# Kernel optimization log

Hardware: AMD Instinct MI355X
Metric: run time of the kernel (lower is better)

The kernel has to match this reference:

```python
import jax, jax.numpy as jnp
import numpy as np

N = 100000
NFEAT = 128
NHID = 16
HEADS = 8
NCLASS = 40
E = 1600000
NEG_SLOPE = 0.2  # PyG GATConv default


def glorot(key, shape):
    fan = shape[0] + shape[-1]
    limit = float(np.sqrt(6.0 / fan))
    return jax.random.uniform(key, shape, jnp.float32, -limit, limit)


def setup_inputs() -> dict:
    key = jax.random.key(0)
    ks = jax.random.split(key, 10)
    x = jax.random.normal(ks[0], (N, NFEAT), jnp.float32)
    adj = jnp.zeros((1,), jnp.float32)  # unused by forward, kept for signature parity
    edge_index = jax.random.randint(ks[1], (2, E), 0, N, jnp.int64)
    # layer 1: GATConv(NFEAT, NHID, heads=HEADS)
    W1 = glorot(ks[2], (NFEAT, HEADS * NHID))
    att_src1 = glorot(ks[3], (HEADS, NHID))
    att_dst1 = glorot(ks[4], (HEADS, NHID))
    b1 = jnp.zeros((HEADS * NHID,), jnp.float32)
    # layer 2: GATConv(HEADS*NHID, NCLASS, heads=1)
    W2 = glorot(ks[5], (HEADS * NHID, NCLASS))
    att_src2 = glorot(ks[6], (1, NCLASS))
    att_dst2 = glorot(ks[7], (1, NCLASS))
    b2 = jnp.zeros((NCLASS,), jnp.float32)
    return {"x": x, "adj": adj, "edge_index": edge_index,
            "W1": W1, "att_src1": att_src1, "att_dst1": att_dst1, "b1": b1,
            "W2": W2, "att_src2": att_src2, "att_dst2": att_dst2, "b2": b2}


def gat_conv(x, W, att_src, att_dst, bias, src, dst, heads, out_ch):
    n = x.shape[0]
    h = (x @ W).reshape(n, heads, out_ch)              # [N,H,C]
    a_src = (h * att_src[None]).sum(-1)                # [N,H]
    a_dst = (h * att_dst[None]).sum(-1)                # [N,H]
    e = jax.nn.leaky_relu(a_src[src] + a_dst[dst], NEG_SLOPE)  # [E,H]
    # softmax over incoming edges of each destination node
    m = jax.ops.segment_max(e, dst, num_segments=n)
    e = jnp.exp(e - m[dst])
    s = jax.ops.segment_sum(e, dst, num_segments=n)
    alpha = e / s[dst]                                  # [E,H]
    msg = h[src] * alpha[:, :, None]                    # [E,H,C]
    out = jax.ops.segment_sum(msg, dst, num_segments=n)  # [N,H,C]
    return out.reshape(n, heads * out_ch) + bias


def reference(x, adj, edge_index, W1, att_src1, att_dst1, b1, W2, att_src2, att_dst2, b2):
    # PyG GATConv adds self-loops by default
    loops = jnp.arange(N, dtype=edge_index.dtype)
    src = jnp.concatenate([edge_index[0], loops])
    dst = jnp.concatenate([edge_index[1], loops])
    # eval mode: F.dropout is identity
    h = jax.nn.elu(gat_conv(x, W1, att_src1, att_dst1, b1, src, dst, HEADS, NHID))
    h = jax.nn.elu(gat_conv(h, W2, att_src2, att_dst2, b2, src, dst, 1, NCLASS))
    return jax.nn.log_softmax(h, axis=1)
```

## Files before the change

### kernel.cpp

```cpp
#include <hip/hip_runtime.h>
#include <stdint.h>

#define NEG_SLOPE 0.2f

__device__ __forceinline__ float lrelu(float v) { return v >= 0.f ? v : NEG_SLOPE * v; }
__device__ __forceinline__ float elu(float v) { return v > 0.f ? v : expm1f(v); }
__device__ __forceinline__ float pexp(float v) { return __expf(lrelu(v)); }

typedef _Float16 h16x2 __attribute__((ext_vector_type(2)));
typedef _Float16 half8 __attribute__((ext_vector_type(8)));
typedef float floatx4 __attribute__((ext_vector_type(4)));

__device__ __forceinline__ void fma_h2(float& a0, float& a1, float p, unsigned u) {
    h16x2 h = __builtin_bit_cast(h16x2, u);
    a0 += p * (float)h[0];
    a1 += p * (float)h[1];
}


#define HC 1024

__global__ __launch_bounds__(256) void hist_wt_kernel(const int* __restrict__ ei,
                                                      int* __restrict__ deg,
                                                      unsigned* __restrict__ rankd,
                                                      const float* __restrict__ W1,
                                                      const float* __restrict__ W2,
                                                      _Float16* __restrict__ w1t,
                                                      _Float16* __restrict__ w2t,
                                                      int E, int n, int sz) {
    const int b = blockIdx.x;
    const int tid = threadIdx.x;
    if (b < 64) {
        int t = b * 256 + tid;
        int col = t >> 7, k = t & 127;
        w1t[col * 128 + k] = (_Float16)W1[k * 128 + col];
        return;
    }
    if (b < 88) {
        int t = (b - 64) * 256 + tid;
        if (t < 48 * 128) {
            int col = t >> 7, k = t & 127;
            w2t[t] = (col < 40) ? (_Float16)W2[k * 40 + col] : (_Float16)0.f;
        }
        return;
    }
    const int hb = b - 88;
    const int c = hb >> 3, r = hb & 7;
    const int lo = r * sz;
    const int hi = (lo + sz < n) ? lo + sz : n;
    const bool last = (r == 7);
    const int base = c * HC;
    #pragma unroll
    for (int i = 0; i < 4; i++) {
        int e = base + i * 256 + tid;
        if (e >= E) break;
        int d = ei[E + e];
        if (d >= lo && d < hi) {
            unsigned rk = (unsigned)atomicAdd(&deg[d], 1);
            rankd[e] = ((unsigned)d << 7) | rk;
        } else if (last && (unsigned)d >= (unsigned)n) {
            rankd[e] = 0xFFFFFFFFu;
        }
    }
}


#define SCAN_T 256
#define SCAN_TILE 1024

__global__ __launch_bounds__(SCAN_T) void scan_p1_kernel(const int* __restrict__ deg,
                                                         int* __restrict__ bsum, int n) {
    __shared__ int red[SCAN_T];
    int t = threadIdx.x;
    int base = blockIdx.x * SCAN_TILE + t * 4;
    int s = 0;
    #pragma unroll
    for (int i = 0; i < 4; i++) {
        int idx = base + i;
        if (idx < n) s += deg[idx];
    }
    red[t] = s;
    __syncthreads();
    for (int off = SCAN_T / 2; off; off >>= 1) {
        if (t < off) red[t] += red[t + off];
        __syncthreads();
    }
    if (t == 0) bsum[blockIdx.x] = red[0];
}

__global__ __launch_bounds__(SCAN_T) void scan_p3f_kernel(const int* __restrict__ deg,
                                                          const int* __restrict__ bsum,
                                                          int* __restrict__ row_ptr,
                                                          int n, int nbk) {
    __shared__ int red[SCAN_T];
    int t = threadIdx.x;
    red[t] = (t < nbk && t < blockIdx.x) ? bsum[t] : 0;
    __syncthreads();
    for (int off = SCAN_T / 2; off; off >>= 1) {
        if (t < off) red[t] += red[t + off];
        __syncthreads();
    }
    const int blockoff = red[0];
    __syncthreads();

    int base = blockIdx.x * SCAN_TILE + t * 4;
    int v[4];
    int s = 0;
    #pragma unroll
    for (int i = 0; i < 4; i++) {
        int idx = base + i;
        v[i] = (idx < n) ? deg[idx] : 0;
        s += v[i];
    }
    red[t] = s;
    __syncthreads();
    for (int off = 1; off < SCAN_T; off <<= 1) {
        int add = (t >= off) ? red[t - off] : 0;
        __syncthreads();
        red[t] += add;
        __syncthreads();
    }
    int excl = red[t] - s + blockoff;
    #pragma unroll
    for (int i = 0; i < 4; i++) {
        int idx = base + i;
        if (idx < n) row_ptr[idx] = excl;
        excl += v[i];
        if (idx == n - 1) row_ptr[n] = excl;
    }
}

__global__ void scatter_kernel(const int* __restrict__ ei, const unsigned* __restrict__ rankd,
                               const int* __restrict__ row_ptr,
                               int* __restrict__ csr_src, int E) {
    int e = blockIdx.x * blockDim.x + threadIdx.x;
    if (e >= E) return;
    unsigned rd = rankd[e];
    if (rd == 0xFFFFFFFFu) return;
    csr_src[row_ptr[rd >> 7] + (int)(rd & 127u)] = ei[e];
}


__global__ __launch_bounds__(256) void gemm1_mfma_kernel(
    const float* __restrict__ x, const _Float16* __restrict__ w1t,
    const float* __restrict__ as1, const float* __restrict__ ad1,
    _Float16* __restrict__ h1h, float* __restrict__ a1s, float* __restrict__ a1d, int n) {
    __shared__ __align__(16) char Wl[32768];
    const int tid = threadIdx.x;
    {
        const uint4* Wg = (const uint4*)w1t;
        #pragma unroll
        for (int i = 0; i < 8; i++) {
            int it = tid + i * 256;
            uint4 v = Wg[it];
            int b = it * 16;
            *(uint4*)&Wl[b ^ (((b >> 8) & 7) << 4)] = v;
        }
    }
    const int wave = tid >> 6, lane = tid & 63;
    const int cl = lane & 15, g = lane >> 4;
    const int wbase = blockIdx.x * 64 + wave * 16;

    int arow = wbase + cl;
    if (arow >= n) arow = n - 1;
    half8 afr[4];
    #pragma unroll
    for (int t = 0; t < 4; t++) {
        const float4 v0 = *(const float4*)&x[(size_t)arow * 128 + 32 * t + g * 8];
        const float4 v1 = *(const float4*)&x[(size_t)arow * 128 + 32 * t + g * 8 + 4];
        afr[t][0] = (_Float16)v0.x; afr[t][1] = (_Float16)v0.y;
        afr[t][2] = (_Float16)v0.z; afr[t][3] = (_Float16)v0.w;
        afr[t][4] = (_Float16)v1.x; afr[t][5] = (_Float16)v1.y;
        afr[t][6] = (_Float16)v1.z; afr[t][7] = (_Float16)v1.w;
    }
    __syncthreads();

    #pragma unroll
    for (int ct = 0; ct < 8; ct++) {
        const int col = ct * 16 + cl;
        half8 bfr[4];
        #pragma unroll
        for (int t = 0; t < 4; t++) {
            int b = (col << 8) + 64 * t + 16 * g;
            bfr[t] = *(half8*)&Wl[b ^ ((col & 7) << 4)];
        }
        floatx4 acc = {0.f, 0.f, 0.f, 0.f};
        #pragma unroll
        for (int t = 0; t < 4; t++)
            acc = __builtin_amdgcn_mfma_f32_16x16x32_f16(afr[t], bfr[t], acc, 0, 0, 0);
        const float av = as1[col], dv = ad1[col];
        #pragma unroll
        for (int i = 0; i < 4; i++) {
            int r = wbase + g * 4 + i;
            float hv = acc[i];
            if (r < n) h1h[(size_t)r * 128 + col] = (_Float16)hv;
            float ps = hv * av, pd = hv * dv;
            ps += __shfl_xor(ps, 1); ps += __shfl_xor(ps, 2);
            ps += __shfl_xor(ps, 4); ps += __shfl_xor(ps, 8);
            pd += __shfl_xor(pd, 1); pd += __shfl_xor(pd, 2);
            pd += __shfl_xor(pd, 4); pd += __shfl_xor(pd, 8);
            if (cl == 0 && r < n) {
                a1s[r * 8 + ct] = ps;
                a1d[r * 8 + ct] = pd;
            }
        }
    }
}

__global__ __launch_bounds__(256) void agg1_kernel(const int* __restrict__ row_ptr,
                                                   const int* __restrict__ csr_src,
                                                   const float* __restrict__ a1s,
                                                   const float* __restrict__ a1d,
                                                   const uint4* __restrict__ h1q,
                                                   const float* __restrict__ b1,
                                                   _Float16* __restrict__ h2h, int n) {
    int lane = threadIdx.x & 63;
    int d = blockIdx.x * 4 + (threadIdx.x >> 6);
    if (d >= n) return;
    const int g = lane >> 4;
    const int q = lane & 15;
    const int h = q >> 1;
    const float adh = a1d[d * 8 + h];

    float acc[8];
    #pragma unroll
    for (int i = 0; i < 8; i++) acc[i] = 0.f;
    float sum = 0.f;
    if (g == 0) {
        uint4 w = h1q[(size_t)d * 16 + q];
        float ps = pexp(a1s[d * 8 + h] + adh);
        fma_h2(acc[0], acc[1], ps, w.x);
        fma_h2(acc[2], acc[3], ps, w.y);
        fma_h2(acc[4], acc[5], ps, w.z);
        fma_h2(acc[6], acc[7], ps, w.w);
        sum = ps;
    }
    int beg = row_ptr[d], end = row_ptr[d + 1];
    int e = beg + g;
    for (; e + 12 < end; e += 16) {
        int s0 = csr_src[e],     s1 = csr_src[e + 4];
        int s2 = csr_src[e + 8], s3 = csr_src[e + 12];
        uint4 w0 = h1q[(size_t)s0 * 16 + q];
        uint4 w1 = h1q[(size_t)s1 * 16 + q];
        uint4 w2 = h1q[(size_t)s2 * 16 + q];
        uint4 w3 = h1q[(size_t)s3 * 16 + q];
        float p0 = pexp(a1s[s0 * 8 + h] + adh);
        float p1 = pexp(a1s[s1 * 8 + h] + adh);
        float p2 = pexp(a1s[s2 * 8 + h] + adh);
        float p3 = pexp(a1s[s3 * 8 + h] + adh);
        fma_h2(acc[0], acc[1], p0, w0.x); fma_h2(acc[2], acc[3], p0, w0.y);
        fma_h2(acc[4], acc[5], p0, w0.z); fma_h2(acc[6], acc[7], p0, w0.w);
        fma_h2(acc[0], acc[1], p1, w1.x); fma_h2(acc[2], acc[3], p1, w1.y);
        fma_h2(acc[4], acc[5], p1, w1.z); fma_h2(acc[6], acc[7], p1, w1.w);
        fma_h2(acc[0], acc[1], p2, w2.x); fma_h2(acc[2], acc[3], p2, w2.y);
        fma_h2(acc[4], acc[5], p2, w2.z); fma_h2(acc[6], acc[7], p2, w2.w);
        fma_h2(acc[0], acc[1], p3, w3.x); fma_h2(acc[2], acc[3], p3, w3.y);
        fma_h2(acc[4], acc[5], p3, w3.z); fma_h2(acc[6], acc[7], p3, w3.w);
        sum += (p0 + p1) + (p2 + p3);
    }
    for (; e + 4 < end; e += 8) {
        int s0 = csr_src[e], s1 = csr_src[e + 4];
        uint4 w0 = h1q[(size_t)s0 * 16 + q];
        uint4 w1 = h1q[(size_t)s1 * 16 + q];
        float p0 = pexp(a1s[s0 * 8 + h] + adh);
        float p1 = pexp(a1s[s1 * 8 + h] + adh);
        fma_h2(acc[0], acc[1], p0, w0.x); fma_h2(acc[2], acc[3], p0, w0.y);
        fma_h2(acc[4], acc[5], p0, w0.z); fma_h2(acc[6], acc[7], p0, w0.w);
        fma_h2(acc[0], acc[1], p1, w1.x); fma_h2(acc[2], acc[3], p1, w1.y);
        fma_h2(acc[4], acc[5], p1, w1.z); fma_h2(acc[6], acc[7], p1, w1.w);
        sum += p0 + p1;
    }
    for (; e < end; e += 4) {
        int s = csr_src[e];
        uint4 w = h1q[(size_t)s * 16 + q];
        float p = pexp(a1s[s * 8 + h] + adh);
        fma_h2(acc[0], acc[1], p, w.x);
        fma_h2(acc[2], acc[3], p, w.y);
        fma_h2(acc[4], acc[5], p, w.z);
        fma_h2(acc[6], acc[7], p, w.w);
        sum += p;
    }
    sum += __shfl_xor(sum, 16); sum += __shfl_xor(sum, 32);
    #pragma unroll
    for (int i = 0; i < 8; i++) {
        acc[i] += __shfl_xor(acc[i], 16);
        acc[i] += __shfl_xor(acc[i], 32);
    }
    if (g == 0) {
        float rs = 1.f / sum;
        float4 b0 = *(const float4*)&b1[8 * q];
        float4 b4 = *(const float4*)&b1[8 * q + 4];
        half8 o;
        o[0] = (_Float16)elu(acc[0] * rs + b0.x);
        o[1] = (_Float16)elu(acc[1] * rs + b0.y);
        o[2] = (_Float16)elu(acc[2] * rs + b0.z);
        o[3] = (_Float16)elu(acc[3] * rs + b0.w);
        o[4] = (_Float16)elu(acc[4] * rs + b4.x);
        o[5] = (_Float16)elu(acc[5] * rs + b4.y);
        o[6] = (_Float16)elu(acc[6] * rs + b4.z);
        o[7] = (_Float16)elu(acc[7] * rs + b4.w);
        *(half8*)&h2h[(size_t)d * 128 + 8 * q] = o;
    }
}


__global__ __launch_bounds__(256) void gemm2_mfma_kernel(
    const _Float16* __restrict__ h2h, const _Float16* __restrict__ w2t,
    const float* __restrict__ as2, const float* __restrict__ ad2,
    _Float16* __restrict__ h3pk, float* __restrict__ a2d, int n) {
    const int tid = threadIdx.x;
    const int wave = tid >> 6, lane = tid & 63;
    const int cl = lane & 15, g = lane >> 4;
    const int wbase = blockIdx.x * 64 + wave * 16;

    int arow = wbase + cl;
    if (arow >= n) arow = n - 1;
    half8 afr[4];
    #pragma unroll
    for (int t = 0; t < 4; t++)
        afr[t] = *(const half8*)&h2h[(size_t)arow * 128 + 32 * t + 8 * g];

    float ps[4] = {0.f, 0.f, 0.f, 0.f};
    float pd[4] = {0.f, 0.f, 0.f, 0.f};
    #pragma unroll
    for (int ct = 0; ct < 3; ct++) {
        const int col = ct * 16 + cl;
        half8 bfr[4];
        #pragma unroll
        for (int t = 0; t < 4; t++)
            bfr[t] = *(const half8*)&w2t[col * 128 + 32 * t + 8 * g];
        floatx4 acc = {0.f, 0.f, 0.f, 0.f};
        #pragma unroll
        for (int t = 0; t < 4; t++)
            acc = __builtin_amdgcn_mfma_f32_16x16x32_f16(afr[t], bfr[t], acc, 0, 0, 0);
        const bool cv = (col < 40);
        const float av = cv ? as2[col] : 0.f;
        const float dv = cv ? ad2[col] : 0.f;
        #pragma unroll
        for (int i = 0; i < 4; i++) {
            int r = wbase + g * 4 + i;
            float hv = acc[i];
            if (cv && r < n)
                h3pk[(size_t)r * 64 + 2 + col] = (_Float16)hv;
            ps[i] += hv * av;
            pd[i] += hv * dv;
        }
    }
    #pragma unroll
    for (int i = 0; i < 4; i++) {
        float s = ps[i], dd = pd[i];
        s += __shfl_xor(s, 1); s += __shfl_xor(s, 2);
        s += __shfl_xor(s, 4); s += __shfl_xor(s, 8);
        dd += __shfl_xor(dd, 1); dd += __shfl_xor(dd, 2);
        dd += __shfl_xor(dd, 4); dd += __shfl_xor(dd, 8);
        int r = wbase + g * 4 + i;
        if (cl == 0 && r < n) {
            ((float*)h3pk)[(size_t)r * 32] = s;
            a2d[r] = dd;
        }
    }
}

__global__ __launch_bounds__(256) void agg2_final_kernel(const int* __restrict__ row_ptr,
                                                         const int* __restrict__ csr_src,
                                                         const unsigned* __restrict__ h3u,
                                                         const float* __restrict__ a2d,
                                                         const float* __restrict__ b2,
                                                         float* __restrict__ out, int n) {
    const float* h3a = (const float*)h3u;
    int lane = threadIdx.x & 63;
    int d = blockIdx.x * 4 + (threadIdx.x >> 6);
    if (d >= n) return;
    const int g = lane >> 5;
    const int q = lane & 31;
    const bool act = (q < 20);
    const float adh = a2d[d];

    h16x2 hsel = {(_Float16)0.f, (_Float16)0.f};
    if (act && g == 0) hsel = __builtin_bit_cast(h16x2, h3u[(size_t)d * 32 + 1 + q]);

    float acc0 = 0.f, acc1 = 0.f, sum = 0.f;
    if (g == 0) {
        float ps = pexp(h3a[(size_t)d * 32] + adh);
        acc0 = ps * (float)hsel[0]; acc1 = ps * (float)hsel[1]; sum = ps;
    }
    int beg = row_ptr[d], end = row_ptr[d + 1];
    int e = beg + g;
    for (; e + 6 < end; e += 8) {
        int s0 = csr_src[e],     s1 = csr_src[e + 2];
        int s2 = csr_src[e + 4], s3 = csr_src[e + 6];
        float a0 = h3a[(size_t)s0 * 32], a1 = h3a[(size_t)s1 * 32];
        float a2 = h3a[(size_t)s2 * 32], a3 = h3a[(size_t)s3 * 32];
        unsigned w0 = 0u, w1 = 0u, w2 = 0u, w3 = 0u;
        if (act) {
            w0 = h3u[(size_t)s0 * 32 + 1 + q]; w1 = h3u[(size_t)s1 * 32 + 1 + q];
            w2 = h3u[(size_t)s2 * 32 + 1 + q]; w3 = h3u[(size_t)s3 * 32 + 1 + q];
        }
        float p0 = pexp(a0 + adh), p1 = pexp(a1 + adh);
        float p2 = pexp(a2 + adh), p3 = pexp(a3 + adh);
        fma_h2(acc0, acc1, p0, w0);
        fma_h2(acc0, acc1, p1, w1);
        fma_h2(acc0, acc1, p2, w2);
        fma_h2(acc0, acc1, p3, w3);
        sum += (p0 + p1) + (p2 + p3);
    }
    for (; e + 2 < end; e += 4) {
        int s0 = csr_src[e], s1 = csr_src[e + 2];
        float a0 = h3a[(size_t)s0 * 32], a1 = h3a[(size_t)s1 * 32];
        unsigned w0 = 0u, w1 = 0u;
        if (act) {
            w0 = h3u[(size_t)s0 * 32 + 1 + q];
            w1 = h3u[(size_t)s1 * 32 + 1 + q];
        }
        float p0 = pexp(a0 + adh), p1 = pexp(a1 + adh);
        fma_h2(acc0, acc1, p0, w0);
        fma_h2(acc0, acc1, p1, w1);
        sum += p0 + p1;
    }
    for (; e < end; e += 2) {
        int s = csr_src[e];
        float pe = pexp(h3a[(size_t)s * 32] + adh);
        unsigned w = act ? h3u[(size_t)s * 32 + 1 + q] : 0u;
        fma_h2(acc0, acc1, pe, w);
        sum += pe;
    }
    sum += __shfl_xor(sum, 32);
    acc0 += __shfl_xor(acc0, 32);
    acc1 += __shfl_xor(acc1, 32);

    float rs = 1.f / sum;
    float v0 = -3.0e38f, v1 = -3.0e38f;
    if (act) {
        v0 = elu(acc0 * rs + b2[2 * q]);
        v1 = elu(acc1 * rs + b2[2 * q + 1]);
    }
    float mx = (act && g == 0) ? fmaxf(v0, v1) : -3.0e38f;
    #pragma unroll
    for (int off = 32; off; off >>= 1) mx = fmaxf(mx, __shfl_xor(mx, off, 64));
    float es = (act && g == 0) ? (__expf(v0 - mx) + __expf(v1 - mx)) : 0.f;
    #pragma unroll
    for (int off = 32; off; off >>= 1) es += __shfl_xor(es, off, 64);
    if (act && g == 0) {
        float ls = logf(es);
        float2 o;
        o.x = v0 - mx - ls;
        o.y = v1 - mx - ls;
        *(float2*)&out[(size_t)d * 40 + 2 * q] = o;
    }
}

extern "C" void kernel_launch(void* const* d_in, const int* in_sizes, int n_in,
                              void* d_out, int out_size, void* d_ws, size_t ws_size,
                              hipStream_t stream) {
    const float* x   = (const float*)d_in[0];
    const int*   ei  = (const int*)d_in[2];
    const float* W1  = (const float*)d_in[3];
    const float* as1 = (const float*)d_in[4];
    const float* ad1 = (const float*)d_in[5];
    const float* b1  = (const float*)d_in[6];
    const float* W2  = (const float*)d_in[7];
    const float* as2 = (const float*)d_in[8];
    const float* ad2 = (const float*)d_in[9];
    const float* b2  = (const float*)d_in[10];
    float* out = (float*)d_out;

    const int n = in_sizes[0] / 128;
    const int E = in_sizes[2] / 2;
    const int nb = (n + SCAN_TILE - 1) / SCAN_TILE;
    const int nbc = (E + HC - 1) / HC;
    const int sz = (n + 7) / 8;

    float* ws = (float*)d_ws;
    _Float16* h1h = (_Float16*)ws;
    _Float16* h2h = (_Float16*)(ws + (size_t)n * 64);
    float* A  = ws + (size_t)n * 128;
    int* deg    = (int*)A;
    int* bsum   = deg + n;
    float* a1s = A;
    float* a1d = A + (size_t)n * 8;
    float* a2d = A;
    int* row_ptr = (int*)(A + (size_t)n * 16);
    int* csr_src = row_ptr + (n + 1);
    unsigned* rankd = (unsigned*)(csr_src + E);
    _Float16* w1t = (_Float16*)(((uintptr_t)(rankd + E) + 63) & ~(uintptr_t)63);
    _Float16* w2t = w1t + 128 * 128;
    _Float16* h3pk = h1h;

    hipMemsetAsync(deg, 0, (size_t)n * sizeof(int), stream);
    hist_wt_kernel<<<88 + nbc * 8, 256, 0, stream>>>(ei, deg, rankd, W1, W2,
                                                     w1t, w2t, E, n, sz);
    scan_p1_kernel<<<nb, SCAN_T, 0, stream>>>(deg, bsum, n);
    scan_p3f_kernel<<<nb, SCAN_T, 0, stream>>>(deg, bsum, row_ptr, n, nb);
    scatter_kernel<<<(E + 255) / 256, 256, 0, stream>>>(ei, rankd, row_ptr, csr_src, E);

    gemm1_mfma_kernel<<<(n + 63) / 64, 256, 0, stream>>>(x, w1t, as1, ad1, h1h, a1s, a1d, n);
    agg1_kernel<<<(n + 3) / 4, 256, 0, stream>>>(row_ptr, csr_src, a1s, a1d,
                                                 (const uint4*)h1h, b1, h2h, n);

    gemm2_mfma_kernel<<<(n + 63) / 64, 256, 0, stream>>>(h2h, w2t, as2, ad2, h3pk, a2d, n);
    agg2_final_kernel<<<(n + 3) / 4, 256, 0, stream>>>(row_ptr, csr_src, (const unsigned*)h3pk,
                                                       a2d, b2, out, n);
}
```

Measured before the change: 413.3 us.

## Move destination-range partitioning from histogram to CSR scatter kernel

The histogram kernel now processes each edge once with a plain atomicAdd instead of eight passes partitioned by destination range. The scatter kernel instead takes the 8-way destination partitioning, with each block reading four edges through vector loads and writing only those whose destination falls in its slice. This is meant to improve the locality of the row_ptr gathers and csr_src writes, and to shrink the histogram launch. The cost is that the scatter now reads rankd and ei eight times, atomics in the histogram lose range locality, and the vector loads assume E is a multiple of 4 (rankd is realigned to 16 bytes for this).

Result: no change. 413.4 us (+0.0%).

```diff
diff --git a/kernel.cpp b/kernel.cpp
--- a/kernel.cpp
+++ b/kernel.cpp
@@ -17,8 +17,6 @@
     a1 += p * (float)h[1];
 }
 
-
-#define HC 1024
 
 __global__ __launch_bounds__(256) void hist_wt_kernel(const int* __restrict__ ei,
                                                       int* __restrict__ deg,
@@ -27,7 +25,7 @@
                                                       const float* __restrict__ W2,
                                                       _Float16* __restrict__ w1t,
                                                       _Float16* __restrict__ w2t,
-                                                      int E, int n, int sz) {
+                                                      int E, int n) {
     const int b = blockIdx.x;
     const int tid = threadIdx.x;
     if (b < 64) {
@@ -44,24 +42,13 @@
         }
         return;
     }
-    const int hb = b - 88;
-    const int c = hb >> 3, r = hb & 7;
-    const int lo = r * sz;
-    const int hi = (lo + sz < n) ? lo + sz : n;
-    const bool last = (r == 7);
-    const int base = c * HC;
-    #pragma unroll
-    for (int i = 0; i < 4; i++) {
-        int e = base + i * 256 + tid;
-        if (e >= E) break;
-        int d = ei[E + e];
-        if (d >= lo && d < hi) {
-            unsigned rk = (unsigned)atomicAdd(&deg[d], 1);
-            rankd[e] = ((unsigned)d << 7) | rk;
-        } else if (last && (unsigned)d >= (unsigned)n) {
-            rankd[e] = 0xFFFFFFFFu;
-        }
-    }
+    int e = (b - 88) * 256 + tid;
+    if (e >= E) return;
+    int d = ei[E + e];
+    unsigned rd = 0xFFFFFFFFu;
+    if ((unsigned)d < (unsigned)n)
+        rd = ((unsigned)d << 7) | (unsigned)atomicAdd(&deg[d], 1);
+    rankd[e] = rd;
 }
 
 
@@ -130,14 +117,34 @@
     }
 }
 
-__global__ void scatter_kernel(const int* __restrict__ ei, const unsigned* __restrict__ rankd,
-                               const int* __restrict__ row_ptr,
-                               int* __restrict__ csr_src, int E) {
-    int e = blockIdx.x * blockDim.x + threadIdx.x;
-    if (e >= E) return;
-    unsigned rd = rankd[e];
-    if (rd == 0xFFFFFFFFu) return;
-    csr_src[row_ptr[rd >> 7] + (int)(rd & 127u)] = ei[e];
+
+#define SC 1024
+
+__global__ __launch_bounds__(256) void scatter8_kernel(const int* __restrict__ ei,
+                                                       const unsigned* __restrict__ rankd,
+                                                       const int* __restrict__ row_ptr,
+                                                       int* __restrict__ csr_src,
+                                                       int E, int sz) {
+    const int hb = blockIdx.x;
+    const int c = hb >> 3, r = hb & 7;
+    const int lo = r * sz, hi = lo + sz;
+    int e0 = c * SC + threadIdx.x * 4;
+    if (e0 >= E) return;
+    uint4 r4 = *(const uint4*)&rankd[e0];
+    int4 s4 = *(const int4*)&ei[e0];
+    int d;
+    d = (int)(r4.x >> 7);
+    if (r4.x != 0xFFFFFFFFu && d >= lo && d < hi)
+        csr_src[row_ptr[d] + (int)(r4.x & 127u)] = s4.x;
+    d = (int)(r4.y >> 7);
+    if (r4.y != 0xFFFFFFFFu && d >= lo && d < hi)
+        csr_src[row_ptr[d] + (int)(r4.y & 127u)] = s4.y;
+    d = (int)(r4.z >> 7);
+    if (r4.z != 0xFFFFFFFFu && d >= lo && d < hi)
+        csr_src[row_ptr[d] + (int)(r4.z & 127u)] = s4.z;
+    d = (int)(r4.w >> 7);
+    if (r4.w != 0xFFFFFFFFu && d >= lo && d < hi)
+        csr_src[row_ptr[d] + (int)(r4.w & 127u)] = s4.w;
 }
 
 
@@ -467,7 +474,8 @@
     const int n = in_sizes[0] / 128;
     const int E = in_sizes[2] / 2;
     const int nb = (n + SCAN_TILE - 1) / SCAN_TILE;
-    const int nbc = (E + HC - 1) / HC;
+    const int nbh = (E + 255) / 256;
+    const int nsc = (E + SC - 1) / SC;
     const int sz = (n + 7) / 8;
 
     float* ws = (float*)d_ws;
@@ -481,17 +489,17 @@
     float* a2d = A;
     int* row_ptr = (int*)(A + (size_t)n * 16);
     int* csr_src = row_ptr + (n + 1);
-    unsigned* rankd = (unsigned*)(csr_src + E);
+    unsigned* rankd = (unsigned*)(((uintptr_t)(csr_src + E) + 15) & ~(uintptr_t)15);
     _Float16* w1t = (_Float16*)(((uintptr_t)(rankd + E) + 63) & ~(uintptr_t)63);
     _Float16* w2t = w1t + 128 * 128;
     _Float16* h3pk = h1h;
 
     hipMemsetAsync(deg, 0, (size_t)n * sizeof(int), stream);
-    hist_wt_kernel<<<88 + nbc * 8, 256, 0, stream>>>(ei, deg, rankd, W1, W2,
-                                                     w1t, w2t, E, n, sz);
+    hist_wt_kernel<<<88 + nbh, 256, 0, stream>>>(ei, deg, rankd, W1, W2,
+                                                 w1t, w2t, E, n);
     scan_p1_kernel<<<nb, SCAN_T, 0, stream>>>(deg, bsum, n);
     scan_p3f_kernel<<<nb, SCAN_T, 0, stream>>>(deg, bsum, row_ptr, n, nb);
-    scatter_kernel<<<(E + 255) / 256, 256, 0, stream>>>(ei, rankd, row_ptr, csr_src, E);
+    scatter8_kernel<<<nsc * 8, 256, 0, stream>>>(ei, rankd, row_ptr, csr_src, E, sz);
 
     gemm1_mfma_kernel<<<(n + 63) / 64, 256, 0, stream>>>(x, w1t, as1, ad1, h1h, a1s, a1d, n);
     agg1_kernel<<<(n + 3) / 4, 256, 0, stream>>>(row_ptr, csr_src, a1s, a1d,
```
